# Kernel optimization log

Hardware: AMD Instinct MI355X
Metric: run time of the kernel (lower is better)

Reference implementation:

```python
import jax, jax.numpy as jnp
import numpy as np

N, E, G = 50000, 400000, 64
IN_CH, HID, H, EDGE_DIM = 128, 64, 4, 4
NEG_SLOPE = 0.2


def setup_inputs() -> dict:
    key = jax.random.key(0)
    ks = list(jax.random.split(key, 40))
    kit = iter(ks)

    def rn(shape, scale=0.05):
        return jax.random.normal(next(kit), shape, dtype=jnp.float32) * scale

    inp = {
        "x": jax.random.normal(next(kit), (N, IN_CH), dtype=jnp.float32),
        "edge_attr": jax.random.uniform(next(kit), (E, 2), dtype=jnp.float32),
        "edge_index": jax.random.randint(next(kit), (2, E), 0, N),
        "batch": jnp.sort(jax.random.randint(next(kit), (N,), 0, G)),
    }
    # edge feature fusion MLPs
    inp["W_et"] = rn((1, EDGE_DIM // 2)); inp["b_et"] = jnp.zeros((EDGE_DIM // 2,), jnp.float32)
    inp["W_uw"] = rn((1, EDGE_DIM // 2)); inp["b_uw"] = jnp.zeros((EDGE_DIM // 2,), jnp.float32)
    inp["W_ua"] = rn((1, 1));             inp["b_ua"] = jnp.zeros((1,), jnp.float32)
    # two GATv2 layers
    for li, ic in ((0, IN_CH), (1, HID)):
        inp[f"Wl{li}"] = rn((ic, H * HID)); inp[f"bl{li}"] = jnp.zeros((H * HID,), jnp.float32)
        inp[f"Wr{li}"] = rn((ic, H * HID)); inp[f"br{li}"] = jnp.zeros((H * HID,), jnp.float32)
        inp[f"att{li}"] = rn((H, HID))
        inp[f"We{li}"] = rn((EDGE_DIM, H * HID))
        inp[f"bias{li}"] = jnp.zeros((HID,), jnp.float32)
    # heads
    inp["W_fc"] = rn((HID, HID)); inp["b_fc"] = jnp.zeros((HID,), jnp.float32)
    inp["W_res"] = rn((HID, 1)); inp["b_res"] = jnp.zeros((1,), jnp.float32)
    inp["W_time"] = rn((HID, 1)); inp["b_time"] = jnp.zeros((1,), jnp.float32)
    return inp


def gatv2_layer(x, src, dst, edge_attr_proj, Wl, bl, Wr, br, att, We, bias):
    # GATv2Conv, concat=False (mean over heads)
    xl = (x @ Wl + bl).reshape(-1, H, HID)   # [N,H,C] transformed source feats
    xr = (x @ Wr + br).reshape(-1, H, HID)   # [N,H,C] transformed target feats
    ee = (edge_attr_proj @ We).reshape(-1, H, HID)  # [E,H,C]
    xj = xl[src]                              # per-edge gather of source
    m = jax.nn.leaky_relu(xj + xr[dst] + ee, NEG_SLOPE)  # [E,H,C]
    score = jnp.einsum('ehc,hc->eh', m, att)  # [E,H]
    # segment softmax over incoming edges of each destination node
    smax = jax.ops.segment_max(score, dst, num_segments=N)  # [N,H]
    ex = jnp.exp(score - smax[dst])
    denom = jax.ops.segment_sum(ex, dst, num_segments=N)
    alpha = ex / (denom[dst] + 1e-16)         # [E,H]
    out = jax.ops.segment_sum(xj * alpha[..., None], dst, num_segments=N)  # [N,H,C]
    return out.mean(axis=1) + bias            # [N,C]


def reference(x, edge_attr, W_et, b_et, W_uw, b_uw, W_ua, b_ua,
              Wl0, bl0, Wr0, br0, att0, We0, bias0,
              Wl1, bl1, Wr1, br1, att1, We1, bias1,
              W_fc, b_fc, W_res, b_res, W_time, b_time,
              edge_index, batch):
    src, dst = edge_index[0], edge_index[1]
    edge_type = edge_attr[:, 0:1]
    unwind = edge_attr[:, 1:2]
    et_emb = edge_type @ W_et + b_et
    uw_emb = unwind @ W_uw + b_uw
    uw_att = jax.nn.sigmoid(unwind @ W_ua + b_ua)
    eap = jnp.concatenate([et_emb, uw_emb * uw_att], axis=-1)  # [E,4]

    h = jax.nn.relu(gatv2_layer(x, src, dst, eap, Wl0, bl0, Wr0, br0, att0, We0, bias0))
    h = jax.nn.relu(gatv2_layer(h, src, dst, eap, Wl1, bl1, Wr1, br1, att1, We1, bias1))

    # global mean pool over graphs (dropout is identity at inference)
    sums = jax.ops.segment_sum(h, batch, num_segments=G)
    cnts = jax.ops.segment_sum(jnp.ones((h.shape[0],), h.dtype), batch, num_segments=G)
    pooled = sums / jnp.maximum(cnts, 1.0)[:, None]
    g = jax.nn.relu(pooled @ W_fc + b_fc)
    result = g @ W_res + b_res
    time = g @ W_time + b_time
    return jnp.concatenate([result, time], axis=1)  # [G,2]
```

## Files before the change

kernel.cpp:

```cpp
#include <hip/hip_runtime.h>
#include <math.h>

namespace {

constexpr int N = 50000;
constexpr int E = 400000;
constexpr int G = 64;
constexpr int HID = 64;
constexpr int HH = 256;
constexpr int NCT = 32;
constexpr float NEG = 0.2f;
constexpr int GAT_BLOCKS = 2048;
constexpr int GAT_WAVES = GAT_BLOCKS * 4;

constexpr int NPROJ = (N + 31) / 32;
constexpr int PH1 = 782;
constexpr int PH1_ROWS = PH1 * 32;
constexpr int PH2 = NPROJ - PH1;
constexpr int HIST_BLOCKS = (E + 255) / 256;
constexpr int PACK_BLOCKS = 52;
constexpr int ZERO_ELEMS = G * HID + N;
constexpr int ZERO_BLOCKS = (ZERO_ELEMS + 255) / 256;

typedef __attribute__((ext_vector_type(8))) short short8v;
typedef __attribute__((ext_vector_type(4))) float f32x4;

__device__ __forceinline__ unsigned short f2bf(float f) {
    unsigned int u = __float_as_uint(f);
    u += 0x7FFFu + ((u >> 16) & 1u);
    return (unsigned short)(u >> 16);
}
__device__ __forceinline__ float bf2f(unsigned short h) {
    return __uint_as_float(((unsigned int)h) << 16);
}
__device__ __forceinline__ float4 ld_bf4(const unsigned short* p) {
    uint2 u = *(const uint2*)p;
    float4 r;
    r.x = __uint_as_float(u.x << 16);
    r.y = __uint_as_float(u.x & 0xFFFF0000u);
    r.z = __uint_as_float(u.y << 16);
    r.w = __uint_as_float(u.y & 0xFFFF0000u);
    return r;
}

__global__ __launch_bounds__(256) void prep_k(
    const float* __restrict__ Wl0, const float* __restrict__ Wr0,
    const float* __restrict__ bl0, const float* __restrict__ br0,
    const float* __restrict__ Wl1, const float* __restrict__ Wr1,
    const float* __restrict__ bl1, const float* __restrict__ br1,
    unsigned short* __restrict__ w0hi, unsigned short* __restrict__ w0lo,
    unsigned short* __restrict__ w1hi, unsigned short* __restrict__ w1lo,
    float* __restrict__ bc0, float* __restrict__ bc1,
    int* __restrict__ zero_base)
{
    int b = blockIdx.x;
    if (b >= PACK_BLOCKS) {
        int i = (b - PACK_BLOCKS) * 256 + threadIdx.x;
        if (i < ZERO_ELEMS) zero_base[i] = 0;
        return;
    }
    int idx = b * 256 + threadIdx.x;
    if (idx < 8192) {
        int lane = idx & 63, ct = (idx >> 6) & 31, kt = idx >> 11;
        int col = ct * 16 + (lane & 15);
        const float* W = (col < 256) ? Wl0 : Wr0;
        int c = col & 255;
        int kb = kt * 32 + ((lane >> 4) & 3) * 8;
#pragma unroll
        for (int e = 0; e < 8; e++) {
            float v = W[(size_t)(kb + e) * 256 + c];
            unsigned short hi = f2bf(v);
            unsigned short lo = f2bf(v - bf2f(hi));
            w0hi[(size_t)idx * 8 + e] = hi;
            w0lo[(size_t)idx * 8 + e] = lo;
        }
    } else if (idx < 8192 + 4096) {
        int s = idx - 8192;
        int lane = s & 63, ct = (s >> 6) & 31, kt = s >> 11;
        int col = ct * 16 + (lane & 15);
        const float* W = (col < 256) ? Wl1 : Wr1;
        int c = col & 255;
        int kb = kt * 32 + ((lane >> 4) & 3) * 8;
#pragma unroll
        for (int e = 0; e < 8; e++) {
            float v = W[(size_t)(kb + e) * 256 + c];
            unsigned short hi = f2bf(v);
            unsigned short lo = f2bf(v - bf2f(hi));
            w1hi[(size_t)s * 8 + e] = hi;
            w1lo[(size_t)s * 8 + e] = lo;
        }
    } else if (idx < 8192 + 4096 + 512) {
        int i = idx - (8192 + 4096);
        bc0[i] = (i < 256) ? bl0[i] : br0[i - 256];
    } else if (idx < 8192 + 4096 + 1024) {
        int i = idx - (8192 + 4096 + 512);
        bc1[i] = (i < 256) ? bl1[i] : br1[i - 256];
    }
}

template <int IC>
__device__ __forceinline__ void proj_body(
    int base,
    const float* __restrict__ x,
    const unsigned short* __restrict__ whi, const unsigned short* __restrict__ wlo,
    const float* __restrict__ bc,
    unsigned short* __restrict__ xlb, unsigned short* __restrict__ xrb)
{
    constexpr int KT = IC / 32;
    constexpr int LDX = IC + 4;
    constexpr int SROW = 516;
    constexpr int XS_BYTES = 32 * LDX * 4;
    constexpr int ST_BYTES = 16 * SROW * 2;
    constexpr int SMEM_BYTES = (XS_BYTES > ST_BYTES) ? XS_BYTES : ST_BYTES;
    __shared__ char smem[SMEM_BYTES];
    float (*xs)[LDX] = (float (*)[LDX])smem;
    const int tid = threadIdx.x;
    for (int idx = tid; idx < 32 * IC / 4; idx += 256) {
        int j = idx / (IC / 4), k4 = idx - j * (IC / 4);
        int n = base + j;
        float4 v = make_float4(0.f, 0.f, 0.f, 0.f);
        if (n < N) v = *(const float4*)&x[(size_t)n * IC + k4 * 4];
        *(float4*)&xs[j][k4 * 4] = v;
    }
    __syncthreads();
    const int w = tid >> 6, lane = tid & 63;
    const int lr = lane & 15, lg = lane >> 4;
    f32x4 acc[2][8];
#pragma unroll
    for (int rt = 0; rt < 2; rt++)
#pragma unroll
        for (int ct = 0; ct < 8; ct++) {
            f32x4 z = {0.f, 0.f, 0.f, 0.f};
            acc[rt][ct] = z;
        }
#pragma unroll
    for (int kt = 0; kt < KT; kt++) {
        short8v ahi[2], alo[2];
#pragma unroll
        for (int rt = 0; rt < 2; rt++) {
            const float* p = &xs[rt * 16 + lr][kt * 32 + lg * 8];
            float4 v0 = *(const float4*)p;
            float4 v1 = *(const float4*)(p + 4);
            float fv[8] = {v0.x, v0.y, v0.z, v0.w, v1.x, v1.y, v1.z, v1.w};
            short8v h, l;
#pragma unroll
            for (int e = 0; e < 8; e++) {
                unsigned short hb = f2bf(fv[e]);
                h[e] = (short)hb;
                l[e] = (short)f2bf(fv[e] - bf2f(hb));
            }
            ahi[rt] = h;
            alo[rt] = l;
        }
        const size_t bbase = ((size_t)(kt * NCT + w * 8) * 64 + lane) * 8;
#pragma unroll
        for (int ct = 0; ct < 8; ct++) {
            short8v bhi = *(const short8v*)&whi[bbase + (size_t)ct * 64 * 8];
            short8v blo = *(const short8v*)&wlo[bbase + (size_t)ct * 64 * 8];
#pragma unroll
            for (int rt = 0; rt < 2; rt++) {
                acc[rt][ct] = __builtin_amdgcn_mfma_f32_16x16x32_bf16(ahi[rt], bhi, acc[rt][ct], 0, 0, 0);
                acc[rt][ct] = __builtin_amdgcn_mfma_f32_16x16x32_bf16(alo[rt], bhi, acc[rt][ct], 0, 0, 0);
                acc[rt][ct] = __builtin_amdgcn_mfma_f32_16x16x32_bf16(ahi[rt], blo, acc[rt][ct], 0, 0, 0);
            }
        }
    }
    __syncthreads();
    unsigned short* st = (unsigned short*)smem;
#pragma unroll
    for (int rt = 0; rt < 2; rt++) {
#pragma unroll
        for (int ct = 0; ct < 8; ct++) {
            int col = (w * 8 + ct) * 16 + lr;
            float bv = bc[col];
            f32x4 a = acc[rt][ct];
#pragma unroll
            for (int i = 0; i < 4; i++) {
                st[(lg * 4 + i) * SROW + col] = f2bf(a[i] + bv);
            }
        }
        __syncthreads();
        int rbase = base + rt * 16;
#pragma unroll
        for (int k = 0; k < 4; k++) {
            int ci = tid + k * 256;
            int rl = ci >> 6;
            int cc = (ci & 63) * 8;
            int rg = rbase + rl;
            if (rg < N) {
                uint2 lo = *(const uint2*)&st[rl * SROW + cc];
                uint2 hi = *(const uint2*)&st[rl * SROW + cc + 4];
                uint4 val = make_uint4(lo.x, lo.y, hi.x, hi.y);
                if (cc < 256) *(uint4*)&xlb[(size_t)rg * HH + cc] = val;
                else          *(uint4*)&xrb[(size_t)rg * HH + (cc - 256)] = val;
            }
        }
        __syncthreads();
    }
}

__global__ __launch_bounds__(256) void k1_projhist_k(
    const float* __restrict__ x,
    const unsigned short* __restrict__ whi, const unsigned short* __restrict__ wlo,
    const float* __restrict__ bc,
    unsigned short* __restrict__ xlb, unsigned short* __restrict__ xrb,
    const int* __restrict__ dst, int* __restrict__ deg, int* __restrict__ rank)
{
    if (blockIdx.x < PH1) {
        proj_body<128>(blockIdx.x * 32, x, whi, wlo, bc, xlb, xrb);
    } else {
        int e = (blockIdx.x - PH1) * 256 + threadIdx.x;
        if (e < E) rank[e] = atomicAdd(&deg[dst[e]], 1);
    }
}

__global__ __launch_bounds__(256) void k2_projscan_k(
    const float* __restrict__ x,
    const unsigned short* __restrict__ whi, const unsigned short* __restrict__ wlo,
    const float* __restrict__ bc,
    unsigned short* __restrict__ xlb, unsigned short* __restrict__ xrb,
    const int* __restrict__ deg, int* __restrict__ pre)
{
    if (blockIdx.x < PH2) {
        proj_body<128>(PH1_ROWS + blockIdx.x * 32, x, whi, wlo, bc, xlb, xrb);
    } else {
        constexpr int CH = 196;
        __shared__ int sums[256];
        int t = threadIdx.x;
        int cbase = t * CH;
        int cend = (cbase + CH < N) ? cbase + CH : N;
        int s = 0;
        for (int i = cbase; i < cend; ++i) s += deg[i];
        sums[t] = s;
        __syncthreads();
        for (int off = 1; off < 256; off <<= 1) {
            int tv = (t >= off) ? sums[t - off] : 0;
            __syncthreads();
            sums[t] += tv;
            __syncthreads();
        }
        int run = sums[t] - s;
        for (int i = cbase; i < cend; ++i) {
            pre[i] = run;
            run += deg[i];
        }
    }
}

__global__ __launch_bounds__(256) void scatter_k(
    const int* __restrict__ src, const int* __restrict__ dst,
    const float* __restrict__ ea,
    const float* __restrict__ W_et, const float* __restrict__ b_et,
    const float* __restrict__ W_uw, const float* __restrict__ b_uw,
    const float* __restrict__ W_ua, const float* __restrict__ b_ua,
    const int* __restrict__ pre, const int* __restrict__ rank,
    int* __restrict__ csr_src, float* __restrict__ eap_csr)
{
    int e = blockIdx.x * 256 + threadIdx.x;
    if (e >= E) return;
    float et = ea[e * 2 + 0], uw = ea[e * 2 + 1];
    float ua = 1.f / (1.f + expf(-(uw * W_ua[0] + b_ua[0])));
    float4 v;
    v.x = et * W_et[0] + b_et[0];
    v.y = et * W_et[1] + b_et[1];
    v.z = (uw * W_uw[0] + b_uw[0]) * ua;
    v.w = (uw * W_uw[1] + b_uw[1]) * ua;
    int d = dst[e];
    int pos = pre[d] + rank[e];
    csr_src[pos] = src[e];
    *(float4*)&eap_csr[(size_t)pos * 4] = v;
}

template <int IC>
__global__ __launch_bounds__(256) void projmm_k(
    const float* __restrict__ x,
    const unsigned short* __restrict__ whi, const unsigned short* __restrict__ wlo,
    const float* __restrict__ bc,
    unsigned short* __restrict__ xlb, unsigned short* __restrict__ xrb)
{
    proj_body<IC>(blockIdx.x * 32, x, whi, wlo, bc, xlb, xrb);
}

__global__ __launch_bounds__(256) void gat_aggr_k(
    const unsigned short* __restrict__ xlb, const unsigned short* __restrict__ xrb,
    const float* __restrict__ eap_csr, const float* __restrict__ We,
    const float* __restrict__ att,
    const int* __restrict__ pre, const int* __restrict__ deg,
    const int* __restrict__ csr_src,
    const float* __restrict__ bias, float* __restrict__ hout)
{
    const int lane = threadIdx.x & 63;
    const int c4 = lane * 4;
    const float4 w0 = *(const float4*)&We[0 * HH + c4];
    const float4 w1 = *(const float4*)&We[1 * HH + c4];
    const float4 w2 = *(const float4*)&We[2 * HH + c4];
    const float4 w3 = *(const float4*)&We[3 * HH + c4];
    const float4 av = *(const float4*)&att[c4];
    float4 bb = make_float4(0.f, 0.f, 0.f, 0.f);
    if (lane < 16) bb = *(const float4*)&bias[c4];

    const int wid = __builtin_amdgcn_readfirstlane(blockIdx.x * 4 + (threadIdx.x >> 6));
    constexpr int q = N / GAT_WAVES;
    constexpr int r = N % GAT_WAVES;
    int d0 = wid * q + (wid < r ? wid : r);
    int dcnt = q + (wid < r ? 1 : 0);

    for (int d = d0; d < d0 + dcnt; ++d) {
        int start = pre[d];
        int end = start + deg[d];
        const float4 vr = ld_bf4(&xrb[(size_t)d * HH + c4]);
        float denom = 0.f;
        float ax = 0.f, ay = 0.f, az = 0.f, aw = 0.f;
        int idx = start;
        for (; idx + 4 <= end; idx += 4) {
            int s0 = csr_src[idx], s1 = csr_src[idx + 1];
            int s2 = csr_src[idx + 2], s3 = csr_src[idx + 3];
            float4 a0 = *(const float4*)&eap_csr[(size_t)(idx + 0) * 4];
            float4 a1 = *(const float4*)&eap_csr[(size_t)(idx + 1) * 4];
            float4 a2 = *(const float4*)&eap_csr[(size_t)(idx + 2) * 4];
            float4 a3 = *(const float4*)&eap_csr[(size_t)(idx + 3) * 4];
            float4 vl0 = ld_bf4(&xlb[(size_t)s0 * HH + c4]);
            float4 vl1 = ld_bf4(&xlb[(size_t)s1 * HH + c4]);
            float4 vl2 = ld_bf4(&xlb[(size_t)s2 * HH + c4]);
            float4 vl3 = ld_bf4(&xlb[(size_t)s3 * HH + c4]);
            float p0, p1, p2, p3;
            {
                float q0 = vl0.x + vr.x + a0.x * w0.x + a0.y * w1.x + a0.z * w2.x + a0.w * w3.x;
                float q1 = vl0.y + vr.y + a0.x * w0.y + a0.y * w1.y + a0.z * w2.y + a0.w * w3.y;
                float q2 = vl0.z + vr.z + a0.x * w0.z + a0.y * w1.z + a0.z * w2.z + a0.w * w3.z;
                float q3 = vl0.w + vr.w + a0.x * w0.w + a0.y * w1.w + a0.z * w2.w + a0.w * w3.w;
                q0 = fmaxf(q0, NEG * q0); q1 = fmaxf(q1, NEG * q1);
                q2 = fmaxf(q2, NEG * q2); q3 = fmaxf(q3, NEG * q3);
                p0 = q0 * av.x + q1 * av.y + q2 * av.z + q3 * av.w;
            }
            {
                float q0 = vl1.x + vr.x + a1.x * w0.x + a1.y * w1.x + a1.z * w2.x + a1.w * w3.x;
                float q1 = vl1.y + vr.y + a1.x * w0.y + a1.y * w1.y + a1.z * w2.y + a1.w * w3.y;
                float q2 = vl1.z + vr.z + a1.x * w0.z + a1.y * w1.z + a1.z * w2.z + a1.w * w3.z;
                float q3 = vl1.w + vr.w + a1.x * w0.w + a1.y * w1.w + a1.z * w2.w + a1.w * w3.w;
                q0 = fmaxf(q0, NEG * q0); q1 = fmaxf(q1, NEG * q1);
                q2 = fmaxf(q2, NEG * q2); q3 = fmaxf(q3, NEG * q3);
                p1 = q0 * av.x + q1 * av.y + q2 * av.z + q3 * av.w;
            }
            {
                float q0 = vl2.x + vr.x + a2.x * w0.x + a2.y * w1.x + a2.z * w2.x + a2.w * w3.x;
                float q1 = vl2.y + vr.y + a2.x * w0.y + a2.y * w1.y + a2.z * w2.y + a2.w * w3.y;
                float q2 = vl2.z + vr.z + a2.x * w0.z + a2.y * w1.z + a2.z * w2.z + a2.w * w3.z;
                float q3 = vl2.w + vr.w + a2.x * w0.w + a2.y * w1.w + a2.z * w2.w + a2.w * w3.w;
                q0 = fmaxf(q0, NEG * q0); q1 = fmaxf(q1, NEG * q1);
                q2 = fmaxf(q2, NEG * q2); q3 = fmaxf(q3, NEG * q3);
                p2 = q0 * av.x + q1 * av.y + q2 * av.z + q3 * av.w;
            }
            {
                float q0 = vl3.x + vr.x + a3.x * w0.x + a3.y * w1.x + a3.z * w2.x + a3.w * w3.x;
                float q1 = vl3.y + vr.y + a3.x * w0.y + a3.y * w1.y + a3.z * w2.y + a3.w * w3.y;
                float q2 = vl3.z + vr.z + a3.x * w0.z + a3.y * w1.z + a3.z * w2.z + a3.w * w3.z;
                float q3 = vl3.w + vr.w + a3.x * w0.w + a3.y * w1.w + a3.z * w2.w + a3.w * w3.w;
                q0 = fmaxf(q0, NEG * q0); q1 = fmaxf(q1, NEG * q1);
                q2 = fmaxf(q2, NEG * q2); q3 = fmaxf(q3, NEG * q3);
                p3 = q0 * av.x + q1 * av.y + q2 * av.z + q3 * av.w;
            }
#pragma unroll
            for (int off = 1; off <= 8; off <<= 1) {
                p0 += __shfl_xor(p0, off, 64);
                p1 += __shfl_xor(p1, off, 64);
                p2 += __shfl_xor(p2, off, 64);
                p3 += __shfl_xor(p3, off, 64);
            }
            float e0 = __expf(p0);
            float e1 = __expf(p1);
            float e2 = __expf(p2);
            float e3 = __expf(p3);
            denom += e0 + e1 + e2 + e3;
            ax += e0 * vl0.x + e1 * vl1.x + e2 * vl2.x + e3 * vl3.x;
            ay += e0 * vl0.y + e1 * vl1.y + e2 * vl2.y + e3 * vl3.y;
            az += e0 * vl0.z + e1 * vl1.z + e2 * vl2.z + e3 * vl3.z;
            aw += e0 * vl0.w + e1 * vl1.w + e2 * vl2.w + e3 * vl3.w;
        }
        for (; idx < end; ++idx) {
            int s = csr_src[idx];
            float4 a = *(const float4*)&eap_csr[(size_t)idx * 4];
            float4 vl = ld_bf4(&xlb[(size_t)s * HH + c4]);
            float q0 = vl.x + vr.x + a.x * w0.x + a.y * w1.x + a.z * w2.x + a.w * w3.x;
            float q1 = vl.y + vr.y + a.x * w0.y + a.y * w1.y + a.z * w2.y + a.w * w3.y;
            float q2 = vl.z + vr.z + a.x * w0.z + a.y * w1.z + a.z * w2.z + a.w * w3.z;
            float q3 = vl.w + vr.w + a.x * w0.w + a.y * w1.w + a.z * w2.w + a.w * w3.w;
            q0 = fmaxf(q0, NEG * q0); q1 = fmaxf(q1, NEG * q1);
            q2 = fmaxf(q2, NEG * q2); q3 = fmaxf(q3, NEG * q3);
            float p = q0 * av.x + q1 * av.y + q2 * av.z + q3 * av.w;
#pragma unroll
            for (int off = 1; off <= 8; off <<= 1) p += __shfl_xor(p, off, 64);
            float e = __expf(p);
            denom += e;
            ax += e * vl.x;
            ay += e * vl.y;
            az += e * vl.z;
            aw += e * vl.w;
        }
        float inv = 0.25f / (denom + 1e-16f);
        ax *= inv; ay *= inv; az *= inv; aw *= inv;
        ax += __shfl_xor(ax, 16, 64); ax += __shfl_xor(ax, 32, 64);
        ay += __shfl_xor(ay, 16, 64); ay += __shfl_xor(ay, 32, 64);
        az += __shfl_xor(az, 16, 64); az += __shfl_xor(az, 32, 64);
        aw += __shfl_xor(aw, 16, 64); aw += __shfl_xor(aw, 32, 64);
        if (lane < 16) {
            float4 o;
            o.x = fmaxf(ax + bb.x, 0.f);
            o.y = fmaxf(ay + bb.y, 0.f);
            o.z = fmaxf(az + bb.z, 0.f);
            o.w = fmaxf(aw + bb.w, 0.f);
            *(float4*)&hout[(size_t)d * HID + c4] = o;
        }
    }
}

__global__ __launch_bounds__(256) void pool_k(
    const float* __restrict__ h, const int* __restrict__ batch,
    float* __restrict__ pooled)
{
    constexpr int CH = 16;
    int c = threadIdx.x & 63;
    int chunk = blockIdx.x * 4 + (threadIdx.x >> 6);
    int n0 = chunk * CH;
    if (n0 >= N) return;
    int nend = (n0 + CH < N) ? n0 + CH : N;
    float sum = 0.f;
    int curb = batch[n0];
    for (int n = n0; n < nend; ++n) {
        int b = batch[n];
        if (b != curb) {
            atomicAdd(&pooled[curb * HID + c], sum);
            sum = 0.f; curb = b;
        }
        sum += h[(size_t)n * HID + c];
    }
    atomicAdd(&pooled[curb * HID + c], sum);
}

__global__ __launch_bounds__(64) void head_k(
    const float* __restrict__ pooled, const int* __restrict__ batch,
    const float* __restrict__ W_fc, const float* __restrict__ b_fc,
    const float* __restrict__ W_res, const float* __restrict__ b_res,
    const float* __restrict__ W_time, const float* __restrict__ b_time,
    float* __restrict__ out)
{
    int g = blockIdx.x;
    int c = threadIdx.x;
    int lo = 0, hi = N;
    while (lo < hi) { int mid = (lo + hi) >> 1; if (batch[mid] < g) lo = mid + 1; else hi = mid; }
    int start = lo;
    hi = N;
    while (lo < hi) { int mid = (lo + hi) >> 1; if (batch[mid] < g + 1) lo = mid + 1; else hi = mid; }
    int end = lo;
    float cnt = (float)(end - start);
    float p = pooled[g * HID + c] / fmaxf(cnt, 1.0f);
    __shared__ float ps[HID];
    ps[c] = p;
    __syncthreads();
    float gv = b_fc[c];
    for (int k = 0; k < HID; k++) gv += ps[k] * W_fc[k * HID + c];
    gv = fmaxf(gv, 0.f);
    float r = gv * W_res[c];
    float t = gv * W_time[c];
#pragma unroll
    for (int off = 32; off > 0; off >>= 1) {
        r += __shfl_down(r, off, 64);
        t += __shfl_down(t, off, 64);
    }
    if (c == 0) {
        out[g * 2 + 0] = r + b_res[0];
        out[g * 2 + 1] = t + b_time[0];
    }
}

}

extern "C" void kernel_launch(void* const* d_in, const int* in_sizes, int n_in,
                              void* d_out, int out_size, void* d_ws, size_t ws_size,
                              hipStream_t stream) {
    const float* x         = (const float*)d_in[0];
    const float* edge_attr = (const float*)d_in[1];
    const int*   edge_index= (const int*)d_in[2];
    const int*   batch     = (const int*)d_in[3];
    const float* W_et = (const float*)d_in[4];
    const float* b_et = (const float*)d_in[5];
    const float* W_uw = (const float*)d_in[6];
    const float* b_uw = (const float*)d_in[7];
    const float* W_ua = (const float*)d_in[8];
    const float* b_ua = (const float*)d_in[9];
    const float* Wl0  = (const float*)d_in[10];
    const float* bl0  = (const float*)d_in[11];
    const float* Wr0  = (const float*)d_in[12];
    const float* br0  = (const float*)d_in[13];
    const float* att0 = (const float*)d_in[14];
    const float* We0  = (const float*)d_in[15];
    const float* bias0= (const float*)d_in[16];
    const float* Wl1  = (const float*)d_in[17];
    const float* bl1  = (const float*)d_in[18];
    const float* Wr1  = (const float*)d_in[19];
    const float* br1  = (const float*)d_in[20];
    const float* att1 = (const float*)d_in[21];
    const float* We1  = (const float*)d_in[22];
    const float* bias1= (const float*)d_in[23];
    const float* W_fc = (const float*)d_in[24];
    const float* b_fc = (const float*)d_in[25];
    const float* W_res= (const float*)d_in[26];
    const float* b_res= (const float*)d_in[27];
    const float* W_time=(const float*)d_in[28];
    const float* b_time=(const float*)d_in[29];

    const int* src = edge_index;
    const int* dst = edge_index + E;

    float* ws    = (float*)d_ws;
    unsigned short* xlb  = (unsigned short*)ws;
    float* xr_reg = ws + (size_t)N * HH;
    unsigned short* xrb  = (unsigned short*)xr_reg;
    unsigned short* w0hi = (unsigned short*)xr_reg + (size_t)N * HH;
    unsigned short* w0lo = w0hi + 65536;
    unsigned short* w1hi = w0lo + 65536;
    unsigned short* w1lo = w1hi + 32768;
    float* bc0 = (float*)(w1lo + 32768);
    float* bc1 = bc0 + 512;
    float* h1    = ws  + (size_t)2 * N * HH;
    float* h2    = h1  + (size_t)N * HID;
    float* pooled= h2  + (size_t)N * HID;
    int*   deg      = (int*)(pooled + (size_t)G * HID);
    int*   pre      = deg + N;
    int*   bsum     = pre + N;
    int*   rank     = bsum + 256;
    int*   csr_src  = rank + E;
    float* eap_csr  = (float*)(csr_src + E);

    dim3 b256(256);

    prep_k<<<PACK_BLOCKS + ZERO_BLOCKS, b256, 0, stream>>>(
        Wl0, Wr0, bl0, br0, Wl1, Wr1, bl1, br1,
        w0hi, w0lo, w1hi, w1lo, bc0, bc1, (int*)pooled);

    k1_projhist_k<<<PH1 + HIST_BLOCKS, b256, 0, stream>>>(
        x, w0hi, w0lo, bc0, xlb, xrb, dst, deg, rank);

    k2_projscan_k<<<PH2 + 1, b256, 0, stream>>>(
        x, w0hi, w0lo, bc0, xlb, xrb, deg, pre);

    scatter_k<<<HIST_BLOCKS, b256, 0, stream>>>(
        src, dst, edge_attr, W_et, b_et, W_uw, b_uw, W_ua, b_ua,
        pre, rank, csr_src, eap_csr);

    gat_aggr_k<<<GAT_BLOCKS, b256, 0, stream>>>(
        xlb, xrb, eap_csr, We0, att0, pre, deg, csr_src, bias0, h1);

    projmm_k<64><<<NPROJ, b256, 0, stream>>>(h1, w1hi, w1lo, bc1, xlb, xrb);
    gat_aggr_k<<<GAT_BLOCKS, b256, 0, stream>>>(
        xlb, xrb, eap_csr, We1, att1, pre, deg, csr_src, bias1, h2);

    pool_k<<<((N + 15) / 16 + 3) / 4, b256, 0, stream>>>(h2, batch, pooled);
    head_k<<<G, dim3(64), 0, stream>>>(
        pooled, batch, W_fc, b_fc, W_res, b_res, W_time, b_time, (float*)d_out);
}
```

Measured before the change: 440.2 us.

## Replace single-block serial degree scan with multi-block two-level scan

```diff
diff --git a/kernel.cpp b/kernel.cpp
--- a/kernel.cpp
+++ b/kernel.cpp
@@ -18,6 +18,7 @@
 constexpr int PH1_ROWS = PH1 * 32;
 constexpr int PH2 = NPROJ - PH1;
 constexpr int HIST_BLOCKS = (E + 255) / 256;
+constexpr int NB = (N + 255) / 256;
 constexpr int PACK_BLOCKS = 52;
 constexpr int ZERO_ELEMS = G * HID + N;
 constexpr int ZERO_BLOCKS = (ZERO_ELEMS + 255) / 256;
@@ -214,37 +215,47 @@
     }
 }
 
-__global__ __launch_bounds__(256) void k2_projscan_k(
+__global__ __launch_bounds__(256) void k2_projscan1_k(
     const float* __restrict__ x,
     const unsigned short* __restrict__ whi, const unsigned short* __restrict__ wlo,
     const float* __restrict__ bc,
     unsigned short* __restrict__ xlb, unsigned short* __restrict__ xrb,
-    const int* __restrict__ deg, int* __restrict__ pre)
+    const int* __restrict__ deg, int* __restrict__ pre, int* __restrict__ bsum)
 {
     if (blockIdx.x < PH2) {
         proj_body<128>(PH1_ROWS + blockIdx.x * 32, x, whi, wlo, bc, xlb, xrb);
     } else {
-        constexpr int CH = 196;
-        __shared__ int sums[256];
-        int t = threadIdx.x;
-        int cbase = t * CH;
-        int cend = (cbase + CH < N) ? cbase + CH : N;
-        int s = 0;
-        for (int i = cbase; i < cend; ++i) s += deg[i];
-        sums[t] = s;
+        __shared__ int s[256];
+        int sb = blockIdx.x - PH2;
+        int i = sb * 256 + threadIdx.x;
+        int v = (i < N) ? deg[i] : 0;
+        s[threadIdx.x] = v;
         __syncthreads();
         for (int off = 1; off < 256; off <<= 1) {
-            int tv = (t >= off) ? sums[t - off] : 0;
+            int t = (threadIdx.x >= off) ? s[threadIdx.x - off] : 0;
             __syncthreads();
-            sums[t] += tv;
+            s[threadIdx.x] += t;
             __syncthreads();
         }
-        int run = sums[t] - s;
-        for (int i = cbase; i < cend; ++i) {
-            pre[i] = run;
-            run += deg[i];
-        }
-    }
+        if (i < N) pre[i] = s[threadIdx.x] - v;
+        if (threadIdx.x == 255) bsum[sb] = s[255];
+    }
+}
+
+__global__ __launch_bounds__(256) void scan2_k(int* __restrict__ bsum, int nb)
+{
+    __shared__ int s[256];
+    int tid = threadIdx.x;
+    int v = (tid < nb) ? bsum[tid] : 0;
+    s[tid] = v;
+    __syncthreads();
+    for (int off = 1; off < 256; off <<= 1) {
+        int t = (tid >= off) ? s[tid - off] : 0;
+        __syncthreads();
+        s[tid] += t;
+        __syncthreads();
+    }
+    if (tid < nb) bsum[tid] = s[tid] - v;
 }
 
 __global__ __launch_bounds__(256) void scatter_k(
@@ -253,7 +264,8 @@
     const float* __restrict__ W_et, const float* __restrict__ b_et,
     const float* __restrict__ W_uw, const float* __restrict__ b_uw,
     const float* __restrict__ W_ua, const float* __restrict__ b_ua,
-    const int* __restrict__ pre, const int* __restrict__ rank,
+    const int* __restrict__ pre, const int* __restrict__ bsum,
+    const int* __restrict__ rank,
     int* __restrict__ csr_src, float* __restrict__ eap_csr)
 {
     int e = blockIdx.x * 256 + threadIdx.x;
@@ -266,7 +278,7 @@
     v.z = (uw * W_uw[0] + b_uw[0]) * ua;
     v.w = (uw * W_uw[1] + b_uw[1]) * ua;
     int d = dst[e];
-    int pos = pre[d] + rank[e];
+    int pos = pre[d] + bsum[d >> 8] + rank[e];
     csr_src[pos] = src[e];
     *(float4*)&eap_csr[(size_t)pos * 4] = v;
 }
@@ -285,7 +297,8 @@
     const unsigned short* __restrict__ xlb, const unsigned short* __restrict__ xrb,
     const float* __restrict__ eap_csr, const float* __restrict__ We,
     const float* __restrict__ att,
-    const int* __restrict__ pre, const int* __restrict__ deg,
+    const int* __restrict__ pre, const int* __restrict__ bsum,
+    const int* __restrict__ deg,
     const int* __restrict__ csr_src,
     const float* __restrict__ bias, float* __restrict__ hout)
 {
@@ -306,7 +319,7 @@
     int dcnt = q + (wid < r ? 1 : 0);
 
     for (int d = d0; d < d0 + dcnt; ++d) {
-        int start = pre[d];
+        int start = pre[d] + bsum[d >> 8];
         int end = start + deg[d];
         const float4 vr = ld_bf4(&xrb[(size_t)d * HH + c4]);
         float denom = 0.f;
@@ -541,19 +554,20 @@
     k1_projhist_k<<<PH1 + HIST_BLOCKS, b256, 0, stream>>>(
         x, w0hi, w0lo, bc0, xlb, xrb, dst, deg, rank);
 
-    k2_projscan_k<<<PH2 + 1, b256, 0, stream>>>(
-        x, w0hi, w0lo, bc0, xlb, xrb, deg, pre);
-
+    k2_projscan1_k<<<PH2 + NB, b256, 0, stream>>>(
+        x, w0hi, w0lo, bc0, xlb, xrb, deg, pre, bsum);
+
+    scan2_k<<<1, b256, 0, stream>>>(bsum, NB);
     scatter_k<<<HIST_BLOCKS, b256, 0, stream>>>(
         src, dst, edge_attr, W_et, b_et, W_uw, b_uw, W_ua, b_ua,
-        pre, rank, csr_src, eap_csr);
+        pre, bsum, rank, csr_src, eap_csr);
 
     gat_aggr_k<<<GAT_BLOCKS, b256, 0, stream>>>(
-        xlb, xrb, eap_csr, We0, att0, pre, deg, csr_src, bias0, h1);
+        xlb, xrb, eap_csr, We0, att0, pre, bsum, deg, csr_src, bias0, h1);
 
     projmm_k<64><<<NPROJ, b256, 0, stream>>>(h1, w1hi, w1lo, bc1, xlb, xrb);
     gat_aggr_k<<<GAT_BLOCKS, b256, 0, stream>>>(
-        xlb, xrb, eap_csr, We1, att1, pre, deg, csr_src, bias1, h2);
+        xlb, xrb, eap_csr, We1, att1, pre, bsum, deg, csr_src, bias1, h2);
 
     pool_k<<<((N + 15) / 16 + 3) / 4, b256, 0, stream>>>(h2, batch, pooled);
     head_k<<<G, dim3(64), 0, stream>>>(
```

Result: faster. 372.1 us (median of 2 runs) (-15.5%).
